# Kernel optimization log

Hardware: AMD Instinct MI355X
Metric: run time of the kernel (lower is better)

Reference implementation:

```python
import jax, jax.numpy as jnp
import numpy as np

VOCAB = 50257
E = 1024
CTX = 1024
C = 50
NEG = 10


def setup_inputs() -> dict:
    key = jax.random.key(0)
    ks = jax.random.split(key, 10)
    return {
        "x": jax.random.randint(ks[0], (1,), 0, VOCAB),
        "context": jax.random.randint(ks[1], (C,), 0, VOCAB),
        "neg_samples": jax.random.randint(ks[2], (C, NEG), 0, VOCAB),
        "emb": jax.random.normal(ks[3], (VOCAB, E), jnp.float32) * 0.02,
        "M_w": jax.random.normal(ks[4], (CTX, E), jnp.float32) * 0.02,
        "M_b": jnp.zeros((CTX,), jnp.float32),
        "U_w": jax.random.normal(ks[5], (CTX, 2 * CTX), jnp.float32) * 0.02,
        "U_b": jnp.zeros((CTX,), jnp.float32),
        "W_w": jax.random.normal(ks[6], (CTX, 2 * CTX), jnp.float32) * 0.02,
        "W_b": jnp.zeros((CTX,), jnp.float32),
        "prior_mus": jax.random.normal(ks[7], (VOCAB, CTX), jnp.float32) * 0.02,
        # keep sigmas away from 0 so log(sigma^2) is well-behaved
        "prior_sigmas": jax.random.uniform(ks[8], (VOCAB, CTX), jnp.float32, 0.5, 1.5),
    }


def reference(x, context, neg_samples, emb, M_w, M_b, U_w, U_b, W_w, W_b,
              prior_mus, prior_sigmas):
    c_len = context.shape[0]
    # Rw: Embedding(x) [1,E] repeated to [C,E], then M (Linear E->CTX)
    Rw = emb[x] @ M_w.T + M_b                       # [1, CTX]
    Rw = jnp.broadcast_to(Rw, (c_len, Rw.shape[-1]))  # [C, CTX]
    Rc = emb[context] @ M_w.T + M_b                 # [C, CTX]
    h = jax.nn.relu(jnp.concatenate([Rw, Rc], axis=1)).sum(0)  # [2*CTX]
    mu = U_w @ h + U_b                              # [CTX]
    # NOTE: posterior covariance is diag(sigma), NOT diag(sigma^2)
    sigma = jax.nn.softplus(W_w @ h + W_b)          # [CTX]

    k = mu.shape[0]
    log_det_p = jnp.sum(jnp.log(sigma))

    def kl_post_to(m, s2):
        # KL( N(mu, diag(sigma)) || N(m, diag(s2)) ), batched over leading dims
        return 0.5 * (jnp.sum((sigma + (m - mu) ** 2) / s2 + jnp.log(s2), axis=-1)
                      - k - log_det_p)

    kl_pos = kl_post_to(prior_mus[context], prior_sigmas[context] ** 2)        # [C]
    kl_neg = kl_post_to(prior_mus[neg_samples], prior_sigmas[neg_samples] ** 2)  # [C, NEG]
    likelihood = jnp.maximum(0.0, kl_neg - kl_pos[:, None] + 1.0).sum()
    kl_prior = kl_post_to(prior_mus[x], prior_sigmas[x] ** 2)                  # [1]
    return likelihood - kl_prior
```

## Files before the change

kernel.cpp:

```cpp
#include <hip/hip_runtime.h>
#include <math.h>

#define EDIM 1024
#define CTXDIM 1024
#define H2 2048


__global__ __launch_bounds__(1024) void k_h(
    const float* __restrict__ emb, const float* __restrict__ Mw,
    const float* __restrict__ Mb, const int* __restrict__ x,
    const int* __restrict__ ctx, int C, float* __restrict__ ws)
{
    __shared__ int   idxs[64];
    __shared__ float pacc[16];
    __shared__ float pxs[4];
    const int tid  = threadIdx.x;
    const int w    = tid >> 6;
    const int lane = tid & 63;
    const int c    = w & 3;
    const int g    = w >> 2;
    const int j    = blockIdx.x * 4 + c;

    if (tid <= C) idxs[tid] = (tid == 0) ? x[0] : ctx[tid - 1];

    const float4* mrow = (const float4*)(Mw + (size_t)j * EDIM);
    const float4 mw0 = mrow[lane];
    const float4 mw1 = mrow[lane + 64];
    const float4 mw2 = mrow[lane + 128];
    const float4 mw3 = mrow[lane + 192];
    const float bj = Mb[j];
    __syncthreads();

    float acc = 0.f, px = 0.f;
#pragma unroll 2
    for (int r = g; r <= C; r += 4) {
        const int idx = idxs[r];
        const float4* e4 = (const float4*)(emb + (size_t)idx * EDIM);
        const float4 a  = e4[lane];
        const float4 bb = e4[lane + 64];
        const float4 d  = e4[lane + 128];
        const float4 e  = e4[lane + 192];
        float s = a.x*mw0.x + a.y*mw0.y + a.z*mw0.z + a.w*mw0.w;
        s += bb.x*mw1.x + bb.y*mw1.y + bb.z*mw1.z + bb.w*mw1.w;
        s += d.x*mw2.x + d.y*mw2.y + d.z*mw2.z + d.w*mw2.w;
        s += e.x*mw3.x + e.y*mw3.y + e.z*mw3.z + e.w*mw3.w;
#pragma unroll
        for (int m = 32; m >= 1; m >>= 1) s += __shfl_xor(s, m);
        const float v = fmaxf(s + bj, 0.f);
        if (r == 0) px = (float)C * v;
        else        acc += v;
    }
    if (lane == 0) {
        pacc[w] = acc;
        if (g == 0) pxs[c] = px;
    }
    __syncthreads();
    if (tid < 4) {
        const int jj = blockIdx.x * 4 + tid;
        ws[jj]          = pxs[tid];
        ws[CTXDIM + jj] = pacc[tid] + pacc[tid + 4] + pacc[tid + 8] + pacc[tid + 12];
    }
}

__global__ __launch_bounds__(512) void k_musig(
    const float* __restrict__ Uw, const float* __restrict__ Ub,
    const float* __restrict__ Ww, const float* __restrict__ Wb,
    float* __restrict__ ws)
{
    if (blockIdx.x == 0 && threadIdx.x == 0) {
        __hip_atomic_store((unsigned*)(ws + 4096) + 2, 0u,
                           __ATOMIC_RELAXED, __HIP_MEMORY_SCOPE_AGENT);
    }
    __shared__ float4 hbuf[512];
    const int tid = threadIdx.x;
    hbuf[tid] = ((const float4*)ws)[tid];
    __syncthreads();

    const int w = tid >> 6, lane = tid & 63;
    const int W = blockIdx.x * 8 + w;
    const bool is_mu = (W < CTXDIM);
    const int rr = W & (CTXDIM - 1);
    const float4* Wr4 = (const float4*)((is_mu ? Uw : Ww) + (size_t)rr * H2);

    float s = 0.f;
#pragma unroll
    for (int k = 0; k < 8; ++k) {
        const float4 wv = Wr4[lane + 64 * k];
        const float4 hv = hbuf[lane + 64 * k];
        s += wv.x*hv.x + wv.y*hv.y + wv.z*hv.z + wv.w*hv.w;
    }
#pragma unroll
    for (int m = 32; m >= 1; m >>= 1) s += __shfl_xor(s, m);

    if (lane == 0) {
        if (is_mu) {
            ws[2048 + rr] = s + Ub[rr];
        } else {
            const float v = s + Wb[rr];
            ws[3072 + rr] = fmaxf(v, 0.f) + log1pf(expf(-fabsf(v)));
        }
    }
}

__global__ __launch_bounds__(256) void k_S(
    const float* __restrict__ pmu, const float* __restrict__ psig,
    const int* __restrict__ x, const int* __restrict__ ctx,
    const int* __restrict__ negs, int C, int CN, int NEG, int KDIM,
    int nblk, float* __restrict__ ws, float* __restrict__ out)
{
    __shared__ float musig[2048];
    const int tid = threadIdx.x;
    float4* ms4 = (float4*)musig;
    ms4[tid]       = ((const float4*)(ws + 2048))[tid];
    ms4[tid + 256] = ((const float4*)(ws + 2048))[tid + 256];
    __syncthreads();

    const int w = tid >> 6, lane = tid & 63;
    const int t = blockIdx.x * 4 + w;
    const int ntask = 2 + C + CN;
    float* Sbuf = ws + 4100;
    unsigned* cnt = (unsigned*)(ws + 4096) + 2;

    if (t < ntask) {
        float acc = 0.f;
        if (t == 0) {
#pragma unroll
            for (int k = 0; k < 16; ++k) acc += logf(musig[1024 + lane + 64 * k]);
        } else {
            int idx;
            if (t == 1)          idx = x[0];
            else if (t < 2 + C)  idx = ctx[t - 2];
            else                 idx = negs[t - 2 - C];
            const float4* m4 = (const float4*)(pmu  + (size_t)idx * CTXDIM);
            const float4* s4 = (const float4*)(psig + (size_t)idx * CTXDIM);
#pragma unroll
            for (int k = 0; k < 4; ++k) {
                const int i = lane + 64 * k;
                const float4 m  = m4[i];
                const float4 sv = s4[i];
                const float4 mu = ms4[i];
                const float4 sg = ms4[256 + i];
                { const float s2 = sv.x*sv.x; const float dd = m.x-mu.x; acc += (sg.x + dd*dd)/s2 + logf(s2); }
                { const float s2 = sv.y*sv.y; const float dd = m.y-mu.y; acc += (sg.y + dd*dd)/s2 + logf(s2); }
                { const float s2 = sv.z*sv.z; const float dd = m.z-mu.z; acc += (sg.z + dd*dd)/s2 + logf(s2); }
                { const float s2 = sv.w*sv.w; const float dd = m.w-mu.w; acc += (sg.w + dd*dd)/s2 + logf(s2); }
            }
        }
#pragma unroll
        for (int m = 32; m >= 1; m >>= 1) acc += __shfl_xor(acc, m);
        if (lane == 0)
            __hip_atomic_store(&Sbuf[t], acc, __ATOMIC_RELAXED, __HIP_MEMORY_SCOPE_AGENT);
    }

    __syncthreads();
    if (w == 0) {
        __builtin_amdgcn_fence(__ATOMIC_RELEASE, "agent");
        int win = 0;
        if (lane == 0) {
            const unsigned old = __hip_atomic_fetch_add(cnt, 1u,
                                   __ATOMIC_RELAXED, __HIP_MEMORY_SCOPE_AGENT);
            win = (old == (unsigned)(nblk - 1));
        }
        win = __shfl(win, 0);
        if (win) {
            __builtin_amdgcn_fence(__ATOMIC_ACQUIRE, "agent");
            float lik = 0.f;
            for (int i = lane; i < CN; i += 64) {
                const float sn = __hip_atomic_load(&Sbuf[2 + C + i],
                                   __ATOMIC_RELAXED, __HIP_MEMORY_SCOPE_AGENT);
                const float sp = __hip_atomic_load(&Sbuf[2 + i / NEG],
                                   __ATOMIC_RELAXED, __HIP_MEMORY_SCOPE_AGENT);
                lik += fmaxf(0.f, 0.5f * (sn - sp) + 1.0f);
            }
#pragma unroll
            for (int m = 32; m >= 1; m >>= 1) lik += __shfl_xor(lik, m);
            if (lane == 0) {
                const float ld = __hip_atomic_load(&Sbuf[0],
                                   __ATOMIC_RELAXED, __HIP_MEMORY_SCOPE_AGENT);
                const float sx = __hip_atomic_load(&Sbuf[1],
                                   __ATOMIC_RELAXED, __HIP_MEMORY_SCOPE_AGENT);
                out[0] = lik - 0.5f * (sx - (float)KDIM - ld);
            }
        }
    }
}

extern "C" void kernel_launch(void* const* d_in, const int* in_sizes, int n_in,
                              void* d_out, int out_size, void* d_ws, size_t ws_size,
                              hipStream_t stream) {
    const int*   x    = (const int*)d_in[0];
    const int*   ctx  = (const int*)d_in[1];
    const int*   negs = (const int*)d_in[2];
    const float* emb  = (const float*)d_in[3];
    const float* Mw   = (const float*)d_in[4];
    const float* Mb   = (const float*)d_in[5];
    const float* Uw   = (const float*)d_in[6];
    const float* Ub   = (const float*)d_in[7];
    const float* Ww   = (const float*)d_in[8];
    const float* Wb   = (const float*)d_in[9];
    const float* pmu  = (const float*)d_in[10];
    const float* psig = (const float*)d_in[11];
    float* ws  = (float*)d_ws;
    float* out = (float*)d_out;

    const int C    = in_sizes[1];
    const int CN   = in_sizes[2];
    const int NEG  = CN / C;
    const int KDIM = in_sizes[5];

    k_h<<<CTXDIM / 4, 1024, 0, stream>>>(emb, Mw, Mb, x, ctx, C, ws);
    k_musig<<<256, 512, 0, stream>>>(Uw, Ub, Ww, Wb, ws);
    const int ntask = 2 + C + CN;
    const int nblk  = (ntask + 3) / 4;
    k_S<<<nblk, 256, 0, stream>>>(pmu, psig, x, ctx, negs,
                                  C, CN, NEG, KDIM, nblk, ws, out);
}
```

Baseline: 25.61 us.

## Fuse mu/sigma GEMV and KL reduction into one column-split tail kernel

```diff
diff --git a/kernel.cpp b/kernel.cpp
--- a/kernel.cpp
+++ b/kernel.cpp
@@ -6,10 +6,12 @@
 #define H2 2048
 
 
+#define ALD(p) __hip_atomic_load((p), __ATOMIC_RELAXED, __HIP_MEMORY_SCOPE_AGENT)
+
 __global__ __launch_bounds__(1024) void k_h(
     const float* __restrict__ emb, const float* __restrict__ Mw,
     const float* __restrict__ Mb, const int* __restrict__ x,
-    const int* __restrict__ ctx, int C, float* __restrict__ ws)
+    const int* __restrict__ ctx, int C, int CN, float* __restrict__ ws)
 {
     __shared__ int   idxs[64];
     __shared__ float pacc[16];
@@ -21,6 +23,8 @@
     const int g    = w >> 2;
     const int j    = blockIdx.x * 4 + c;
 
+    if (blockIdx.x == 0 && tid < 8 + 2 + C + CN)
+        ws[4096 + tid] = 0.f;
     if (tid <= C) idxs[tid] = (tid == 0) ? x[0] : ctx[tid - 1];
 
     const float4* mrow = (const float4*)(Mw + (size_t)j * EDIM);
@@ -62,125 +66,105 @@
     }
 }
 
-__global__ __launch_bounds__(512) void k_musig(
+__global__ __launch_bounds__(1024) void k_tail(
     const float* __restrict__ Uw, const float* __restrict__ Ub,
     const float* __restrict__ Ww, const float* __restrict__ Wb,
-    float* __restrict__ ws)
-{
-    if (blockIdx.x == 0 && threadIdx.x == 0) {
-        __hip_atomic_store((unsigned*)(ws + 4096) + 2, 0u,
-                           __ATOMIC_RELAXED, __HIP_MEMORY_SCOPE_AGENT);
-    }
-    __shared__ float4 hbuf[512];
-    const int tid = threadIdx.x;
-    hbuf[tid] = ((const float4*)ws)[tid];
-    __syncthreads();
-
-    const int w = tid >> 6, lane = tid & 63;
-    const int W = blockIdx.x * 8 + w;
-    const bool is_mu = (W < CTXDIM);
-    const int rr = W & (CTXDIM - 1);
-    const float4* Wr4 = (const float4*)((is_mu ? Uw : Ww) + (size_t)rr * H2);
-
-    float s = 0.f;
-#pragma unroll
-    for (int k = 0; k < 8; ++k) {
-        const float4 wv = Wr4[lane + 64 * k];
-        const float4 hv = hbuf[lane + 64 * k];
-        s += wv.x*hv.x + wv.y*hv.y + wv.z*hv.z + wv.w*hv.w;
-    }
-#pragma unroll
-    for (int m = 32; m >= 1; m >>= 1) s += __shfl_xor(s, m);
-
-    if (lane == 0) {
-        if (is_mu) {
-            ws[2048 + rr] = s + Ub[rr];
-        } else {
-            const float v = s + Wb[rr];
-            ws[3072 + rr] = fmaxf(v, 0.f) + log1pf(expf(-fabsf(v)));
-        }
-    }
-}
-
-__global__ __launch_bounds__(256) void k_S(
     const float* __restrict__ pmu, const float* __restrict__ psig,
     const int* __restrict__ x, const int* __restrict__ ctx,
     const int* __restrict__ negs, int C, int CN, int NEG, int KDIM,
     int nblk, float* __restrict__ ws, float* __restrict__ out)
 {
-    __shared__ float musig[2048];
-    const int tid = threadIdx.x;
-    float4* ms4 = (float4*)musig;
-    ms4[tid]       = ((const float4*)(ws + 2048))[tid];
-    ms4[tid + 256] = ((const float4*)(ws + 2048))[tid + 256];
+    __shared__ float4 hbuf4[512];
+    __shared__ float  msig[16];
+    __shared__ int    winflag;
+    const int tid  = threadIdx.x;
+    const int w    = tid >> 6;
+    const int lane = tid & 63;
+    const int b    = blockIdx.x;
+    float* Sbuf    = ws + 4100;
+    unsigned* cnt  = (unsigned*)(ws + 4096);
+
+    const int nkl = 1 + C + CN;
+    float4 gm0, gm1, gs0, gs1;
+    if (tid < nkl) {
+        const int idx = (tid == 0) ? x[0]
+                       : (tid <= C ? ctx[tid - 1] : negs[tid - 1 - C]);
+        const float4* m4 = (const float4*)(pmu  + (size_t)idx * CTXDIM + 8 * b);
+        const float4* s4 = (const float4*)(psig + (size_t)idx * CTXDIM + 8 * b);
+        gm0 = m4[0]; gm1 = m4[1];
+        gs0 = s4[0]; gs1 = s4[1];
+    }
+
+    if (tid < 512) hbuf4[tid] = ((const float4*)ws)[tid];
     __syncthreads();
 
-    const int w = tid >> 6, lane = tid & 63;
-    const int t = blockIdx.x * 4 + w;
-    const int ntask = 2 + C + CN;
-    float* Sbuf = ws + 4100;
-    unsigned* cnt = (unsigned*)(ws + 4096) + 2;
-
-    if (t < ntask) {
-        float acc = 0.f;
-        if (t == 0) {
+    {
+        const int colw = w & 7;
+        const int i = 8 * b + colw;
+        const float4* W4 = (const float4*)(((w < 8) ? Uw : Ww) + (size_t)i * H2);
+        float s = 0.f;
 #pragma unroll
-            for (int k = 0; k < 16; ++k) acc += logf(musig[1024 + lane + 64 * k]);
-        } else {
-            int idx;
-            if (t == 1)          idx = x[0];
-            else if (t < 2 + C)  idx = ctx[t - 2];
-            else                 idx = negs[t - 2 - C];
-            const float4* m4 = (const float4*)(pmu  + (size_t)idx * CTXDIM);
-            const float4* s4 = (const float4*)(psig + (size_t)idx * CTXDIM);
+        for (int k = 0; k < 8; ++k) {
+            const float4 wv = W4[lane + 64 * k];
+            const float4 hv = hbuf4[lane + 64 * k];
+            s += wv.x*hv.x + wv.y*hv.y + wv.z*hv.z + wv.w*hv.w;
+        }
 #pragma unroll
-            for (int k = 0; k < 4; ++k) {
-                const int i = lane + 64 * k;
-                const float4 m  = m4[i];
-                const float4 sv = s4[i];
-                const float4 mu = ms4[i];
-                const float4 sg = ms4[256 + i];
-                { const float s2 = sv.x*sv.x; const float dd = m.x-mu.x; acc += (sg.x + dd*dd)/s2 + logf(s2); }
-                { const float s2 = sv.y*sv.y; const float dd = m.y-mu.y; acc += (sg.y + dd*dd)/s2 + logf(s2); }
-                { const float s2 = sv.z*sv.z; const float dd = m.z-mu.z; acc += (sg.z + dd*dd)/s2 + logf(s2); }
-                { const float s2 = sv.w*sv.w; const float dd = m.w-mu.w; acc += (sg.w + dd*dd)/s2 + logf(s2); }
+        for (int m = 32; m >= 1; m >>= 1) s += __shfl_xor(s, m);
+        if (lane == 0) {
+            if (w < 8) {
+                msig[colw] = s + Ub[i];
+            } else {
+                const float v = s + Wb[i];
+                msig[8 + colw] = fmaxf(v, 0.f) + log1pf(expf(-fabsf(v)));
             }
         }
+    }
+    __syncthreads();
+
+    if (tid < nkl) {
+        const float mu0 = msig[0], mu1 = msig[1], mu2 = msig[2], mu3 = msig[3];
+        const float mu4 = msig[4], mu5 = msig[5], mu6 = msig[6], mu7 = msig[7];
+        const float sg0 = msig[8], sg1 = msig[9], sg2 = msig[10], sg3 = msig[11];
+        const float sg4 = msig[12], sg5 = msig[13], sg6 = msig[14], sg7 = msig[15];
+        float acc = 0.f;
+        { const float s2 = gs0.x*gs0.x; const float d = gm0.x - mu0; acc += (sg0 + d*d)/s2 + logf(s2); }
+        { const float s2 = gs0.y*gs0.y; const float d = gm0.y - mu1; acc += (sg1 + d*d)/s2 + logf(s2); }
+        { const float s2 = gs0.z*gs0.z; const float d = gm0.z - mu2; acc += (sg2 + d*d)/s2 + logf(s2); }
+        { const float s2 = gs0.w*gs0.w; const float d = gm0.w - mu3; acc += (sg3 + d*d)/s2 + logf(s2); }
+        { const float s2 = gs1.x*gs1.x; const float d = gm1.x - mu4; acc += (sg4 + d*d)/s2 + logf(s2); }
+        { const float s2 = gs1.y*gs1.y; const float d = gm1.y - mu5; acc += (sg5 + d*d)/s2 + logf(s2); }
+        { const float s2 = gs1.z*gs1.z; const float d = gm1.z - mu6; acc += (sg6 + d*d)/s2 + logf(s2); }
+        { const float s2 = gs1.w*gs1.w; const float d = gm1.w - mu7; acc += (sg7 + d*d)/s2 + logf(s2); }
+        atomicAdd(&Sbuf[1 + tid], acc);
+    } else if (tid == nkl) {
+        float ld = 0.f;
 #pragma unroll
-        for (int m = 32; m >= 1; m >>= 1) acc += __shfl_xor(acc, m);
-        if (lane == 0)
-            __hip_atomic_store(&Sbuf[t], acc, __ATOMIC_RELAXED, __HIP_MEMORY_SCOPE_AGENT);
+        for (int jj = 0; jj < 8; ++jj) ld += logf(msig[8 + jj]);
+        atomicAdd(&Sbuf[0], ld);
     }
 
     __syncthreads();
-    if (w == 0) {
-        __builtin_amdgcn_fence(__ATOMIC_RELEASE, "agent");
-        int win = 0;
+    if (tid == 0) {
+        const unsigned old = __hip_atomic_fetch_add(cnt, 1u,
+                               __ATOMIC_RELEASE, __HIP_MEMORY_SCOPE_AGENT);
+        winflag = (old == (unsigned)(nblk - 1));
+    }
+    __syncthreads();
+    if (winflag && w == 0) {
+        __builtin_amdgcn_fence(__ATOMIC_ACQUIRE, "agent");
+        float lik = 0.f;
+        for (int i = lane; i < CN; i += 64) {
+            const float sn = ALD(&Sbuf[2 + C + i]);
+            const float sp = ALD(&Sbuf[2 + i / NEG]);
+            lik += fmaxf(0.f, 0.5f * (sn - sp) + 1.0f);
+        }
+#pragma unroll
+        for (int m = 32; m >= 1; m >>= 1) lik += __shfl_xor(lik, m);
         if (lane == 0) {
-            const unsigned old = __hip_atomic_fetch_add(cnt, 1u,
-                                   __ATOMIC_RELAXED, __HIP_MEMORY_SCOPE_AGENT);
-            win = (old == (unsigned)(nblk - 1));
-        }
-        win = __shfl(win, 0);
-        if (win) {
-            __builtin_amdgcn_fence(__ATOMIC_ACQUIRE, "agent");
-            float lik = 0.f;
-            for (int i = lane; i < CN; i += 64) {
-                const float sn = __hip_atomic_load(&Sbuf[2 + C + i],
-                                   __ATOMIC_RELAXED, __HIP_MEMORY_SCOPE_AGENT);
-                const float sp = __hip_atomic_load(&Sbuf[2 + i / NEG],
-                                   __ATOMIC_RELAXED, __HIP_MEMORY_SCOPE_AGENT);
-                lik += fmaxf(0.f, 0.5f * (sn - sp) + 1.0f);
-            }
-#pragma unroll
-            for (int m = 32; m >= 1; m >>= 1) lik += __shfl_xor(lik, m);
-            if (lane == 0) {
-                const float ld = __hip_atomic_load(&Sbuf[0],
-                                   __ATOMIC_RELAXED, __HIP_MEMORY_SCOPE_AGENT);
-                const float sx = __hip_atomic_load(&Sbuf[1],
-                                   __ATOMIC_RELAXED, __HIP_MEMORY_SCOPE_AGENT);
-                out[0] = lik - 0.5f * (sx - (float)KDIM - ld);
-            }
+            const float ld = ALD(&Sbuf[0]);
+            const float sx = ALD(&Sbuf[1]);
+            out[0] = lik - 0.5f * (sx - (float)KDIM - ld);
         }
     }
 }
@@ -208,10 +192,8 @@
     const int NEG  = CN / C;
     const int KDIM = in_sizes[5];
 
-    k_h<<<CTXDIM / 4, 1024, 0, stream>>>(emb, Mw, Mb, x, ctx, C, ws);
-    k_musig<<<256, 512, 0, stream>>>(Uw, Ub, Ww, Wb, ws);
-    const int ntask = 2 + C + CN;
-    const int nblk  = (ntask + 3) / 4;
-    k_S<<<nblk, 256, 0, stream>>>(pmu, psig, x, ctx, negs,
-                                  C, CN, NEG, KDIM, nblk, ws, out);
+    k_h<<<CTXDIM / 4, 1024, 0, stream>>>(emb, Mw, Mb, x, ctx, C, CN, ws);
+    k_tail<<<CTXDIM / 8, 1024, 0, stream>>>(Uw, Ub, Ww, Wb, pmu, psig,
+                                            x, ctx, negs, C, CN, NEG, KDIM,
+                                            CTXDIM / 8, ws, out);
 }
```

New measurement: 30.19 us. 1.18x slower.

## Fuse mu/sigma and KL kernels with in-kernel grid barrier and prefetch

Applied to the files above, without the earlier changes.

```diff
diff --git a/kernel.cpp b/kernel.cpp
--- a/kernel.cpp
+++ b/kernel.cpp
@@ -5,6 +5,9 @@
 #define CTXDIM 1024
 #define H2 2048
 
+
+#define AST(p, v) __hip_atomic_store((p), (v), __ATOMIC_RELAXED, __HIP_MEMORY_SCOPE_AGENT)
+#define ALD(p)    __hip_atomic_load((p), __ATOMIC_RELAXED, __HIP_MEMORY_SCOPE_AGENT)
 
 __global__ __launch_bounds__(1024) void k_h(
     const float* __restrict__ emb, const float* __restrict__ Mw,
@@ -21,6 +24,10 @@
     const int g    = w >> 2;
     const int j    = blockIdx.x * 4 + c;
 
+    if (blockIdx.x == 0) {
+        ws[4096 + tid] = 0.f;
+        if (tid < 64) ws[5120 + tid] = 0.f;
+    }
     if (tid <= C) idxs[tid] = (tid == 0) ? x[0] : ctx[tid - 1];
 
     const float4* mrow = (const float4*)(Mw + (size_t)j * EDIM);
@@ -62,82 +69,117 @@
     }
 }
 
-__global__ __launch_bounds__(512) void k_musig(
+__global__ __launch_bounds__(512) void k_tail(
     const float* __restrict__ Uw, const float* __restrict__ Ub,
     const float* __restrict__ Ww, const float* __restrict__ Wb,
-    float* __restrict__ ws)
-{
-    if (blockIdx.x == 0 && threadIdx.x == 0) {
-        __hip_atomic_store((unsigned*)(ws + 4096) + 2, 0u,
-                           __ATOMIC_RELAXED, __HIP_MEMORY_SCOPE_AGENT);
-    }
-    __shared__ float4 hbuf[512];
-    const int tid = threadIdx.x;
-    hbuf[tid] = ((const float4*)ws)[tid];
-    __syncthreads();
-
-    const int w = tid >> 6, lane = tid & 63;
-    const int W = blockIdx.x * 8 + w;
-    const bool is_mu = (W < CTXDIM);
-    const int rr = W & (CTXDIM - 1);
-    const float4* Wr4 = (const float4*)((is_mu ? Uw : Ww) + (size_t)rr * H2);
-
-    float s = 0.f;
-#pragma unroll
-    for (int k = 0; k < 8; ++k) {
-        const float4 wv = Wr4[lane + 64 * k];
-        const float4 hv = hbuf[lane + 64 * k];
-        s += wv.x*hv.x + wv.y*hv.y + wv.z*hv.z + wv.w*hv.w;
-    }
-#pragma unroll
-    for (int m = 32; m >= 1; m >>= 1) s += __shfl_xor(s, m);
-
-    if (lane == 0) {
-        if (is_mu) {
-            ws[2048 + rr] = s + Ub[rr];
-        } else {
-            const float v = s + Wb[rr];
-            ws[3072 + rr] = fmaxf(v, 0.f) + log1pf(expf(-fabsf(v)));
-        }
-    }
-}
-
-__global__ __launch_bounds__(256) void k_S(
     const float* __restrict__ pmu, const float* __restrict__ psig,
     const int* __restrict__ x, const int* __restrict__ ctx,
     const int* __restrict__ negs, int C, int CN, int NEG, int KDIM,
-    int nblk, float* __restrict__ ws, float* __restrict__ out)
+    int nsblk, float* __restrict__ ws, float* __restrict__ out)
 {
-    __shared__ float musig[2048];
-    const int tid = threadIdx.x;
-    float4* ms4 = (float4*)musig;
-    ms4[tid]       = ((const float4*)(ws + 2048))[tid];
-    ms4[tid + 256] = ((const float4*)(ws + 2048))[tid + 256];
-    __syncthreads();
-
-    const int w = tid >> 6, lane = tid & 63;
-    const int t = blockIdx.x * 4 + w;
+    __shared__ float smem[2048];
+    __shared__ int   winflag;
+    const int tid  = threadIdx.x;
+    const int w    = tid >> 6;
+    const int lane = tid & 63;
+    const int b    = blockIdx.x;
+    unsigned* bar  = (unsigned*)(ws + 4096);
+    float* Sbuf    = ws + 5248;
+
+    if (b < 256) {
+        float4* hbuf = (float4*)smem;
+        hbuf[tid] = ((const float4*)ws)[tid];
+        __syncthreads();
+
+        const int W = b * 8 + w;
+        const bool is_mu = (W < CTXDIM);
+        const int rr = W & (CTXDIM - 1);
+        const float4* Wr4 = (const float4*)((is_mu ? Uw : Ww) + (size_t)rr * H2);
+        float s = 0.f;
+#pragma unroll
+        for (int k = 0; k < 8; ++k) {
+            const float4 wv = Wr4[lane + 64 * k];
+            const float4 hv = hbuf[lane + 64 * k];
+            s += wv.x*hv.x + wv.y*hv.y + wv.z*hv.z + wv.w*hv.w;
+        }
+#pragma unroll
+        for (int m = 32; m >= 1; m >>= 1) s += __shfl_xor(s, m);
+        if (lane == 0) {
+            if (is_mu) {
+                AST(&ws[2048 + rr], s + Ub[rr]);
+            } else {
+                const float v = s + Wb[rr];
+                AST(&ws[3072 + rr], fmaxf(v, 0.f) + log1pf(expf(-fabsf(v))));
+            }
+        }
+        __syncthreads();
+        if (tid == 0) {
+            const unsigned old = __hip_atomic_fetch_add(&bar[32 * (b & 15)], 1u,
+                                   __ATOMIC_RELAXED, __HIP_MEMORY_SCOPE_AGENT);
+            if (old == 15u) {
+                const unsigned o2 = __hip_atomic_fetch_add(&bar[32 * 16], 1u,
+                                      __ATOMIC_RELAXED, __HIP_MEMORY_SCOPE_AGENT);
+                if (o2 == 15u) {
+#pragma unroll
+                    for (int i = 0; i < 16; ++i)
+                        AST(&bar[32 * (17 + i)], 1u);
+                }
+            }
+        }
+        return;
+    }
+
+    const int t = (b - 256) * 8 + w;
     const int ntask = 2 + C + CN;
-    float* Sbuf = ws + 4100;
-    unsigned* cnt = (unsigned*)(ws + 4096) + 2;
-
-    if (t < ntask) {
+
+    const bool iskl = (t >= 1 && t < ntask);
+    float4 gm[4], gsv[4];
+    if (iskl) {
+        int idx;
+        if (t == 1)          idx = x[0];
+        else if (t < 2 + C)  idx = ctx[t - 2];
+        else                 idx = negs[t - 2 - C];
+        const float4* m4 = (const float4*)(pmu  + (size_t)idx * CTXDIM);
+        const float4* s4 = (const float4*)(psig + (size_t)idx * CTXDIM);
+#pragma unroll
+        for (int k = 0; k < 4; ++k) {
+            gm[k]  = m4[lane + 64 * k];
+            gsv[k] = s4[lane + 64 * k];
+        }
+    }
+
+    if (tid == 0) {
+        while (ALD(&bar[32 * (17 + (b & 15))]) == 0u)
+            __builtin_amdgcn_s_sleep(8);
+    }
+    __syncthreads();
+    __builtin_amdgcn_sched_barrier(0);
+
+    {
+        const unsigned long long* src = (const unsigned long long*)(ws + 2048);
+#pragma unroll
+        for (int q = 0; q < 2; ++q) {
+            const int i = tid + 512 * q;
+            const unsigned long long v = __hip_atomic_load(&src[i],
+                __ATOMIC_RELAXED, __HIP_MEMORY_SCOPE_AGENT);
+            smem[2 * i]     = __uint_as_float((unsigned)(v & 0xffffffffu));
+            smem[2 * i + 1] = __uint_as_float((unsigned)(v >> 32));
+        }
+    }
+    __syncthreads();
+
+    {
         float acc = 0.f;
         if (t == 0) {
 #pragma unroll
-            for (int k = 0; k < 16; ++k) acc += logf(musig[1024 + lane + 64 * k]);
+            for (int k = 0; k < 16; ++k) acc += logf(smem[1024 + lane + 64 * k]);
         } else {
-            int idx;
-            if (t == 1)          idx = x[0];
-            else if (t < 2 + C)  idx = ctx[t - 2];
-            else                 idx = negs[t - 2 - C];
-            const float4* m4 = (const float4*)(pmu  + (size_t)idx * CTXDIM);
-            const float4* s4 = (const float4*)(psig + (size_t)idx * CTXDIM);
+            const float4* ms4 = (const float4*)smem;
 #pragma unroll
             for (int k = 0; k < 4; ++k) {
                 const int i = lane + 64 * k;
-                const float4 m  = m4[i];
-                const float4 sv = s4[i];
+                const float4 m  = gm[k];
+                const float4 sv = gsv[k];
                 const float4 mu = ms4[i];
                 const float4 sg = ms4[256 + i];
                 { const float s2 = sv.x*sv.x; const float dd = m.x-mu.x; acc += (sg.x + dd*dd)/s2 + logf(s2); }
@@ -148,8 +190,7 @@
         }
 #pragma unroll
         for (int m = 32; m >= 1; m >>= 1) acc += __shfl_xor(acc, m);
-        if (lane == 0)
-            __hip_atomic_store(&Sbuf[t], acc, __ATOMIC_RELAXED, __HIP_MEMORY_SCOPE_AGENT);
+        if (lane == 0) AST(&Sbuf[t], acc);
     }
 
     __syncthreads();
@@ -157,28 +198,24 @@
         __builtin_amdgcn_fence(__ATOMIC_RELEASE, "agent");
         int win = 0;
         if (lane == 0) {
-            const unsigned old = __hip_atomic_fetch_add(cnt, 1u,
+            const unsigned old = __hip_atomic_fetch_add(&bar[32 * 33], 1u,
                                    __ATOMIC_RELAXED, __HIP_MEMORY_SCOPE_AGENT);
-            win = (old == (unsigned)(nblk - 1));
+            win = (old == (unsigned)(nsblk - 1));
         }
         win = __shfl(win, 0);
         if (win) {
             __builtin_amdgcn_fence(__ATOMIC_ACQUIRE, "agent");
             float lik = 0.f;
             for (int i = lane; i < CN; i += 64) {
-                const float sn = __hip_atomic_load(&Sbuf[2 + C + i],
-                                   __ATOMIC_RELAXED, __HIP_MEMORY_SCOPE_AGENT);
-                const float sp = __hip_atomic_load(&Sbuf[2 + i / NEG],
-                                   __ATOMIC_RELAXED, __HIP_MEMORY_SCOPE_AGENT);
+                const float sn = ALD(&Sbuf[2 + C + i]);
+                const float sp = ALD(&Sbuf[2 + i / NEG]);
                 lik += fmaxf(0.f, 0.5f * (sn - sp) + 1.0f);
             }
 #pragma unroll
             for (int m = 32; m >= 1; m >>= 1) lik += __shfl_xor(lik, m);
             if (lane == 0) {
-                const float ld = __hip_atomic_load(&Sbuf[0],
-                                   __ATOMIC_RELAXED, __HIP_MEMORY_SCOPE_AGENT);
-                const float sx = __hip_atomic_load(&Sbuf[1],
-                                   __ATOMIC_RELAXED, __HIP_MEMORY_SCOPE_AGENT);
+                const float ld = ALD(&Sbuf[0]);
+                const float sx = ALD(&Sbuf[1]);
                 out[0] = lik - 0.5f * (sx - (float)KDIM - ld);
             }
         }
@@ -208,10 +245,11 @@
     const int NEG  = CN / C;
     const int KDIM = in_sizes[5];
 
+    const int ntask = 2 + C + CN;
+    const int nsblk = (ntask + 7) / 8;
+
     k_h<<<CTXDIM / 4, 1024, 0, stream>>>(emb, Mw, Mb, x, ctx, C, ws);
-    k_musig<<<256, 512, 0, stream>>>(Uw, Ub, Ww, Wb, ws);
-    const int ntask = 2 + C + CN;
-    const int nblk  = (ntask + 3) / 4;
-    k_S<<<nblk, 256, 0, stream>>>(pmu, psig, x, ctx, negs,
-                                  C, CN, NEG, KDIM, nblk, ws, out);
+    k_tail<<<256 + nsblk, 512, 0, stream>>>(Uw, Ub, Ww, Wb, pmu, psig,
+                                            x, ctx, negs, C, CN, NEG, KDIM,
+                                            nsblk, ws, out);
 }
```

Measured after the change: 25.89 us (median of 2 runs). About the same (+1.1%).
